# Optimization experiments

Hardware: AMD Instinct MI355X
Metric: run time of the kernel (lower is better)

Reference implementation:

```python
import jax, jax.numpy as jnp
import numpy as np
import math

B, QLEN, KLEN = 8, 128, 1024
KDIM = QDIM = ADIM = ODIM = 512
HM, HC = 4, 4            # monotonic / chunkwise heads
CHUNK = 4                # chunkwise attention window
EPS = 1e-6
SHARPENING = 1.0
NEG_INF = float(np.finfo(np.float32).min)


def moving_sum(x, back, forward):
    """Windowed sum over last axis: out[k] = sum_{j=k-back}^{k+forward} x[j].
    Equivalent to the conv1d-with-ones-filter moving_sum in the torch code."""
    K = x.shape[-1]
    xp = jnp.pad(x, [(0, 0)] * (x.ndim - 1) + [(back, forward)])
    cs = jnp.cumsum(xp, axis=-1)
    L = back + forward + 1
    upper = jax.lax.slice_in_dim(cs, L - 1, L - 1 + K, axis=-1)
    lower = jnp.concatenate([jnp.zeros_like(cs[..., :1]),
                             jax.lax.slice_in_dim(cs, 0, K - 1, axis=-1)], axis=-1)
    return upper - lower


def safe_cumprod(x, eps):
    """exp(exclusive_cumsum(log(clip(x, eps, 1)))) along last axis."""
    logx = jnp.log(jnp.clip(x, eps, 1.0))
    excl = jnp.concatenate([jnp.zeros_like(logx[..., :1]),
                            jnp.cumsum(logx, axis=-1)[..., :-1]], axis=-1)
    return jnp.exp(excl)


def _heads(x, w, b, h):
    y = x @ w + b                                   # [B, L, ADIM]
    bs, L, _ = y.shape
    return y.reshape(bs, L, h, -1).transpose(0, 2, 1, 3)  # [B, h, L, d_k]


def setup_inputs() -> dict:
    key = jax.random.key(0)
    ks = jax.random.split(key, 16)
    s = 0.02
    f32 = jnp.float32
    return {
        "key_x": jax.random.normal(ks[0], (B, KLEN, KDIM), f32),
        "query_x": jax.random.normal(ks[1], (B, QLEN, QDIM), f32),
        "mask": jnp.ones((B, QLEN, KLEN), jnp.int32),
        "wk_m": jax.random.normal(ks[2], (KDIM, ADIM), f32) * s,
        "bk_m": jnp.zeros((ADIM,), f32),
        "wq_m": jax.random.normal(ks[3], (QDIM, ADIM), f32) * s,
        "bq_m": jnp.zeros((ADIM,), f32),
        "r": jnp.asarray(-4.0, f32),
        "wk_c": jax.random.normal(ks[4], (KDIM, ADIM), f32) * s,
        "bk_c": jnp.zeros((ADIM,), f32),
        "wq_c": jax.random.normal(ks[5], (QDIM, ADIM), f32) * s,
        "bq_c": jnp.zeros((ADIM,), f32),
        "wv": jax.random.normal(ks[6], (KDIM, ADIM), f32) * s,
        "bv": jnp.zeros((ADIM,), f32),
        "wo": jax.random.normal(ks[7], (ADIM, ODIM), f32) * s,
        "bo": jnp.zeros((ODIM,), f32),
    }


def reference(key_x, query_x, mask, wk_m, bk_m, wq_m, bq_m, r,
              wk_c, bk_c, wq_c, bq_c, wv, bv, wo, bo):
    scale = math.sqrt(ADIM)
    m = (mask[:, None] > 0)                                    # [B,1,Q,K]

    # ---- monotonic energy (scaled_dot + offset r) ----
    km = _heads(key_x, wk_m, bk_m, HM)                         # [B,HM,K,dk]
    qm = _heads(query_x, wq_m, bq_m, HM)                       # [B,HM,Q,dk]
    e_mono = jnp.einsum('bhqd,bhkd->bhqk', qm, km) / scale + r
    e_mono = jnp.where(m, e_mono, NEG_INF)

    # ---- monotonic alpha via safe_cumprod + per-step cumsum recurrence ----
    p_choose = jax.nn.sigmoid(e_mono)                          # [B,HM,Q,K]
    cp = safe_cumprod(1.0 - p_choose, EPS)                     # [B,HM,Q,K]
    aw0 = jnp.zeros((B, HM, KLEN), e_mono.dtype).at[..., 0].set(1.0)

    def step(aw_prev, pc):
        p_i, cp_i = pc                                         # [B,HM,K]
        aw = p_i * cp_i * jnp.cumsum(aw_prev / jnp.maximum(cp_i, EPS), axis=-1)
        return aw, aw

    _, alpha = jax.lax.scan(step, aw0,
                            (p_choose.transpose(2, 0, 1, 3),
                             cp.transpose(2, 0, 1, 3)))
    alpha = alpha.transpose(1, 2, 0, 3)                        # [B,HM,Q,K]

    # ---- chunkwise energy ----
    kc = _heads(key_x, wk_c, bk_c, HC)
    qc = _heads(query_x, wq_c, bq_c, HC)
    e_chunk = jnp.einsum('bhqd,bhkd->bhqk', qc, kc) / scale
    e_chunk = jnp.where(m, e_chunk, NEG_INF)

    # ---- efficient chunkwise attention (clipped-logit trick) ----
    e = e_chunk - jnp.max(e_chunk, axis=-1, keepdims=True)
    sexp = jnp.maximum(jnp.exp(e), 1e-5)[:, None]              # [B,1,HC,Q,K]
    denom = moving_sum(sexp, CHUNK - 1, 0)                     # [B,1,HC,Q,K]
    beta = sexp * moving_sum(alpha[:, :, None] * SHARPENING / denom,
                             0, CHUNK - 1)                     # [B,HM,HC,Q,K]
    beta = beta.reshape(B, HM * HC, QLEN, KLEN)

    # ---- context + output projection ----
    v = (key_x @ wv + bv).reshape(B, KLEN, HM * HC, ADIM // (HM * HC))
    cv = jnp.einsum('bhqk,bkhd->bqhd', beta, v).reshape(B, QLEN, ADIM)
    return cv @ wo + bo
```

## Files before the change

kernel.cpp:

```cpp
#include <hip/hip_runtime.h>
#include <hip/hip_bf16.h>


#define NEG_INF (-3.402823466e38f)
#define EPS_MOCHA 1e-6f
#define INV_SCALE 0.04419417382415922f

typedef _Float16 half8 __attribute__((ext_vector_type(8)));
typedef _Float16 half4v __attribute__((ext_vector_type(4)));
typedef float f32x4 __attribute__((ext_vector_type(4)));

#define WAITBAR(N) asm volatile("s_waitcnt vmcnt(" #N ") lgkmcnt(0)\n\ts_barrier" ::: "memory")

__device__ __forceinline__ float wave_incl_scan(float x)
{
    int v;
    v = __builtin_amdgcn_update_dpp(0, __builtin_bit_cast(int, x), 0x111, 0xF, 0xF, false);
    x += __builtin_bit_cast(float, v);
    v = __builtin_amdgcn_update_dpp(0, __builtin_bit_cast(int, x), 0x112, 0xF, 0xF, false);
    x += __builtin_bit_cast(float, v);
    v = __builtin_amdgcn_update_dpp(0, __builtin_bit_cast(int, x), 0x114, 0xF, 0xF, false);
    x += __builtin_bit_cast(float, v);
    v = __builtin_amdgcn_update_dpp(0, __builtin_bit_cast(int, x), 0x118, 0xF, 0xF, false);
    x += __builtin_bit_cast(float, v);
    v = __builtin_amdgcn_update_dpp(0, __builtin_bit_cast(int, x), 0x142, 0xA, 0xF, false);
    x += __builtin_bit_cast(float, v);
    v = __builtin_amdgcn_update_dpp(0, __builtin_bit_cast(int, x), 0x143, 0xC, 0xF, false);
    x += __builtin_bit_cast(float, v);
    return x;
}

__device__ __forceinline__ half8 cvt8(float4 a, float4 b)
{
    half8 h = {(_Float16)a.x, (_Float16)a.y, (_Float16)a.z, (_Float16)a.w,
               (_Float16)b.x, (_Float16)b.y, (_Float16)b.z, (_Float16)b.w};
    return h;
}

__global__ __launch_bounds__(256) void cvt_x(
    const float* __restrict__ key_x, const float* __restrict__ query_x,
    _Float16* __restrict__ X16)
{
    const size_t KELEMS = (size_t)8192 * 512;
    size_t o = ((size_t)blockIdx.x * 256 + threadIdx.x) * 8;
    const float* s = (o < KELEMS) ? (key_x + o) : (query_x + (o - KELEMS));
    float4 a = *(const float4*)s;
    float4 b = *(const float4*)(s + 4);
    *(half8*)(X16 + o) = cvt8(a, b);
}

__global__ __launch_bounds__(256) void prep_weights(
    const float* __restrict__ wk_m, const float* __restrict__ wk_c,
    const float* __restrict__ wv, const float* __restrict__ wq_m,
    const float* __restrict__ wq_c, const float* __restrict__ wo,
    _Float16* __restrict__ Wt5, _Float16* __restrict__ Wt_wo)
{
    __shared__ float T[64][65];
    const int z = blockIdx.z;
    const float* W = (z == 0) ? wk_m : (z == 1) ? wk_c : (z == 2) ? wv
                   : (z == 3) ? wq_m : (z == 4) ? wq_c : wo;
    _Float16* O = (z < 5) ? (Wt5 + (size_t)z * 262144) : Wt_wo;
    const int n0 = blockIdx.x * 64, k0 = blockIdx.y * 64;
    const int t = threadIdx.x;
    const int rr = t >> 4, cc = (t & 15) * 4;
#pragma unroll
    for (int r = 0; r < 4; ++r) {
        int k = r * 16 + rr;
        float4 v = *(const float4*)(W + (size_t)(k0 + k) * 512 + n0 + cc);
        T[k][cc + 0] = v.x; T[k][cc + 1] = v.y;
        T[k][cc + 2] = v.z; T[k][cc + 3] = v.w;
    }
    __syncthreads();
    const int nn = t >> 2, kc = (t & 3) * 16;
    _Float16 tmp[16];
#pragma unroll
    for (int i = 0; i < 16; ++i) tmp[i] = (_Float16)T[kc + i][nn];
    _Float16* Op = O + (size_t)(n0 + nn) * 512 + k0 + kc;
    *(half8*)(Op)     = *(half8*)&tmp[0];
    *(half8*)(Op + 8) = *(half8*)&tmp[8];
}

__device__ __forceinline__ void stage16(const _Float16* src, _Float16* dst)
{
    __builtin_amdgcn_global_load_lds(
        (const __attribute__((address_space(1))) void*)src,
        (__attribute__((address_space(3))) void*)dst, 16, 0, 0);
}

template <int NSTEPS>
__device__ __forceinline__ void gemm8_f16(
    const _Float16* __restrict__ Abase, const _Float16* __restrict__ Bbase,
    _Float16* As, _Float16* Bs, f32x4 acc[4][2])
{
    const int tid = threadIdx.x;
    const int lane = tid & 63, wave = tid >> 6;
    const int wm = wave >> 2, wn = wave & 3;
    const int col = lane & 15, quad = lane >> 4;
    const int r0 = tid >> 2, seg = tid & 3;

    const _Float16* Ag = Abase + (size_t)r0 * 512 + seg * 8;
    const _Float16* Bg = Bbase + (size_t)r0 * 512 + seg * 8;

    stage16(Ag, As + tid * 8);
    stage16(Bg, Bs + tid * 8);
    if (NSTEPS > 1) {
        stage16(Ag + 32, As + 4096 + tid * 8);
        stage16(Bg + 32, Bs + 4096 + tid * 8);
        WAITBAR(2);
    } else {
        WAITBAR(0);
    }

#pragma unroll
    for (int ks = 0; ks < NSTEPS; ++ks) {
        const int cur = ks % 3;
        if (ks + 2 < NSTEPS) {
            const int s2 = (ks + 2) % 3;
            stage16(Ag + (ks + 2) * 32, As + s2 * 4096 + tid * 8);
            stage16(Bg + (ks + 2) * 32, Bs + s2 * 4096 + tid * 8);
        }
        const _Float16* Afr = As + cur * 4096 + (size_t)(wm * 64 + col) * 32 + quad * 8;
        const _Float16* Bfr = Bs + cur * 4096 + (size_t)(wn * 32 + col) * 32 + quad * 8;
        half8 a[4], b[2];
#pragma unroll
        for (int t = 0; t < 4; ++t) a[t] = *(const half8*)(Afr + (size_t)t * 16 * 32);
#pragma unroll
        for (int t = 0; t < 2; ++t) b[t] = *(const half8*)(Bfr + (size_t)t * 16 * 32);
#pragma unroll
        for (int mt = 0; mt < 4; ++mt)
#pragma unroll
            for (int nt = 0; nt < 2; ++nt)
                acc[mt][nt] = __builtin_amdgcn_mfma_f32_16x16x32_f16(
                    a[mt], b[nt], acc[mt][nt], 0, 0, 0);
        if (ks + 2 < NSTEPS)      WAITBAR(2);
        else if (ks + 1 < NSTEPS) WAITBAR(0);
    }
}

__device__ __forceinline__ void proj_epilogue8(
    f32x4 acc[4][2], const float* __restrict__ bias, void* __restrict__ Cv,
    int m0, int n0, int f16o)
{
    const int tid = threadIdx.x;
    const int lane = tid & 63, wave = tid >> 6;
    const int wm = wave >> 2, wn = wave & 3;
    const int col = lane & 15, quad = lane >> 4;
    float bnt[2];
#pragma unroll
    for (int nt = 0; nt < 2; ++nt)
        bnt[nt] = bias[n0 + wn * 32 + nt * 16 + col];
#pragma unroll
    for (int mt = 0; mt < 4; ++mt) {
        const int rowb = m0 + wm * 64 + mt * 16 + quad * 4;
#pragma unroll
        for (int nt = 0; nt < 2; ++nt) {
            const int cc = n0 + wn * 32 + nt * 16 + col;
#pragma unroll
            for (int r = 0; r < 4; ++r) {
                float v = acc[mt][nt][r] + bnt[nt];
                if (f16o)
                    ((_Float16*)Cv)[(size_t)(rowb + r) * 512 + cc] = (_Float16)v;
                else
                    ((float*)Cv)[(size_t)(rowb + r) * 512 + cc] = v;
            }
        }
    }
}

__global__ __launch_bounds__(512, 8) void mfma_proj5(
    const _Float16* __restrict__ X16, const _Float16* __restrict__ Wt5,
    const float* __restrict__ b0, void* __restrict__ C0,
    const float* __restrict__ b1, void* __restrict__ C1,
    const float* __restrict__ b2, void* __restrict__ C2,
    const float* __restrict__ b3, void* __restrict__ C3,
    const float* __restrict__ b4, void* __restrict__ C4)
{
    __shared__ _Float16 As[12288];
    __shared__ _Float16 Bs[12288];
    const int bid = (blockIdx.x & 7) * 104 + (blockIdx.x >> 3);
    int g, mblk, nblk;
    if (bid < 768) {
        g = bid >> 8; mblk = (bid & 255) >> 2; nblk = bid & 3;
    } else {
        const int t = bid - 768;
        g = 3 + (t >> 5); mblk = (t & 31) >> 2; nblk = t & 3;
    }
    const bool qry = g >= 3;
    const _Float16* A = X16 + (qry ? (size_t)8192 * 512 : 0);
    const _Float16* Wt = Wt5 + (size_t)g * 262144;
    const float* bias = (g == 0) ? b0 : (g == 1) ? b1 : (g == 2) ? b2
                      : (g == 3) ? b3 : b4;
    void* Cv = (g == 0) ? C0 : (g == 1) ? C1 : (g == 2) ? C2
             : (g == 3) ? C3 : C4;
    const int f16o = (g == 2) ? 0 : 1;
    const int m0 = mblk * 128, n0 = nblk * 128;

    f32x4 acc[4][2];
#pragma unroll
    for (int mt = 0; mt < 4; ++mt)
#pragma unroll
        for (int nt = 0; nt < 2; ++nt) acc[mt][nt] = (f32x4)0.f;
    gemm8_f16<16>(A + (size_t)m0 * 512, Wt + (size_t)n0 * 512, As, Bs, acc);
    proj_epilogue8(acc, bias, Cv, m0, n0, f16o);
}

__global__ __launch_bounds__(512, 4) void mfma_proj_out(
    const _Float16* __restrict__ A16, const _Float16* __restrict__ Wt,
    const float* __restrict__ bias, float* __restrict__ C)
{
    __shared__ _Float16 As[12288];
    __shared__ _Float16 Bs[12288];
    const int m0 = blockIdx.x * 128, n0 = blockIdx.y * 128;
    f32x4 acc[4][2];
#pragma unroll
    for (int mt = 0; mt < 4; ++mt)
#pragma unroll
        for (int nt = 0; nt < 2; ++nt) acc[mt][nt] = (f32x4)0.f;
    gemm8_f16<16>(A16 + (size_t)m0 * 512, Wt + (size_t)n0 * 512, As, Bs, acc);
    proj_epilogue8(acc, bias, C, m0, n0, 0);
}

__global__ __launch_bounds__(512, 4) void energy_mfma(
    const _Float16* __restrict__ Qm, const _Float16* __restrict__ Km,
    const _Float16* __restrict__ Qc, const _Float16* __restrict__ Kc,
    const int* __restrict__ mask, float* __restrict__ e_mono,
    _Float16* __restrict__ e_chunk16, const float* __restrict__ r_ptr)
{
    __shared__ _Float16 As[12288];
    __shared__ _Float16 Bs[12288];
    const int tid = threadIdx.x;
    const int lane = tid & 63, wave = tid >> 6;
    const int wm = wave >> 2, wn = wave & 3;
    const int col = lane & 15, quad = lane >> 4;
    const int kt0 = blockIdx.x * 128;
    const int h = blockIdx.y;
    const int b = blockIdx.z;
    const float rv = r_ptr[0];
    const int r0 = tid >> 2, seg = tid & 3;

    const _Float16* Am0 = Qm + (size_t)(b * 128) * 512 + h * 128 + (size_t)r0 * 512 + seg * 8;
    const _Float16* Ac0 = Qc + (size_t)(b * 128) * 512 + h * 128 + (size_t)r0 * 512 + seg * 8;
    const _Float16* Bm0 = Km + (size_t)(b * 1024 + kt0) * 512 + h * 128 + (size_t)r0 * 512 + seg * 8;
    const _Float16* Bc0 = Kc + (size_t)(b * 1024 + kt0) * 512 + h * 128 + (size_t)r0 * 512 + seg * 8;
#define EGA(s) (((s) < 4 ? Am0 : Ac0) + ((s) & 3) * 32)
#define EGB(s) (((s) < 4 ? Bm0 : Bc0) + ((s) & 3) * 32)

    f32x4 accM[4][2], accC[4][2];
#pragma unroll
    for (int mt = 0; mt < 4; ++mt)
#pragma unroll
        for (int nt = 0; nt < 2; ++nt) { accM[mt][nt] = (f32x4)0.f; accC[mt][nt] = (f32x4)0.f; }

#pragma unroll
    for (int s = 0; s < 2; ++s) {
        stage16(EGA(s), As + s * 4096 + tid * 8);
        stage16(EGB(s), Bs + s * 4096 + tid * 8);
    }
    WAITBAR(2);

#pragma unroll
    for (int ks = 0; ks < 8; ++ks) {
        const int cur = ks % 3;
        if (ks + 2 < 8) {
            const int s2 = (ks + 2) % 3;
            stage16(EGA(ks + 2), As + s2 * 4096 + tid * 8);
            stage16(EGB(ks + 2), Bs + s2 * 4096 + tid * 8);
        }
        const _Float16* Afr = As + cur * 4096 + (size_t)(wm * 64 + col) * 32 + quad * 8;
        const _Float16* Bfr = Bs + cur * 4096 + (size_t)(wn * 32 + col) * 32 + quad * 8;
        half8 a[4], bf[2];
#pragma unroll
        for (int t = 0; t < 4; ++t) a[t]  = *(const half8*)(Afr + (size_t)t * 16 * 32);
#pragma unroll
        for (int t = 0; t < 2; ++t) bf[t] = *(const half8*)(Bfr + (size_t)t * 16 * 32);
        if (ks < 4) {
#pragma unroll
            for (int mt = 0; mt < 4; ++mt)
#pragma unroll
                for (int nt = 0; nt < 2; ++nt)
                    accM[mt][nt] = __builtin_amdgcn_mfma_f32_16x16x32_f16(a[mt], bf[nt], accM[mt][nt], 0, 0, 0);
        } else {
#pragma unroll
            for (int mt = 0; mt < 4; ++mt)
#pragma unroll
                for (int nt = 0; nt < 2; ++nt)
                    accC[mt][nt] = __builtin_amdgcn_mfma_f32_16x16x32_f16(a[mt], bf[nt], accC[mt][nt], 0, 0, 0);
        }
        if (ks + 2 < 8)      WAITBAR(2);
        else if (ks + 1 < 8) WAITBAR(0);
    }
#undef EGA
#undef EGB

#pragma unroll
    for (int mt = 0; mt < 4; ++mt) {
        const int qb = wm * 64 + mt * 16 + quad * 4;
#pragma unroll
        for (int nt = 0; nt < 2; ++nt) {
            const int kc = kt0 + wn * 32 + nt * 16 + col;
#pragma unroll
            for (int r = 0; r < 4; ++r) {
                const int q = qb + r;
                const int mv = mask[((size_t)b * 128 + q) * 1024 + kc];
                const size_t oi = (((size_t)b * 4 + h) * 128 + q) * 1024 + kc;
                float vm = accM[mt][nt][r] * INV_SCALE + rv;
                e_mono[oi] = mv ? vm : NEG_INF;
                float vc = accC[mt][nt][r] * INV_SCALE;
                e_chunk16[oi] = (_Float16)(mv ? vc : NEG_INF);
            }
        }
    }
}

__device__ __forceinline__ void transcend_row(
    const float* __restrict__ Erow, int lane, float o_pcp[16], float o_inv[16])
{
    const float* E = Erow + lane * 16;
    float e[16];
    *(float4*)&e[0]  = *(const float4*)(E);
    *(float4*)&e[4]  = *(const float4*)(E + 4);
    *(float4*)&e[8]  = *(const float4*)(E + 8);
    *(float4*)&e[12] = *(const float4*)(E + 12);

    float p[16], l[16];
#pragma unroll
    for (int i = 0; i < 16; ++i) {
        p[i] = 1.f / (1.f + expf(-e[i]));
        l[i] = logf(fmaxf(1.f - p[i], EPS_MOCHA));
    }
    float incl[16];
    incl[0] = l[0];
#pragma unroll
    for (int i = 1; i < 16; ++i) incl[i] = incl[i - 1] + l[i];
    float total = incl[15];
    float x = wave_incl_scan(total);
    float base = x - total;
#pragma unroll
    for (int i = 0; i < 16; ++i) {
        float cl = base + (i ? incl[i - 1] : 0.f);
        float cp = expf(cl);
        o_pcp[i] = p[i] * cp;
        o_inv[i] = 1.f / fmaxf(cp, EPS_MOCHA);
    }
}

#define SW2(k) ((k) + ((k) >> 4))

__global__ __launch_bounds__(256) void alpha_pre(
    const float* __restrict__ e_mono, float* __restrict__ G,
    float* __restrict__ pcp)
{
    __shared__ float pshare[4][1088];
    const int tid = threadIdx.x;
    const int lane = tid & 63;
    const int wid = tid >> 6;
    const int row = blockIdx.x * 4 + wid;
    const int q = row & 127;

    float pq[16], iq[16];
    transcend_row(e_mono + (size_t)row * 1024, lane, pq, iq);

    float* P = pcp + (size_t)row * 1024 + lane * 16;
    *(float4*)(P)      = *(float4*)&pq[0];
    *(float4*)(P + 4)  = *(float4*)&pq[4];
    *(float4*)(P + 8)  = *(float4*)&pq[8];
    *(float4*)(P + 12) = *(float4*)&pq[12];

#pragma unroll
    for (int i = 0; i < 16; ++i)
        pshare[wid][SW2(lane * 16 + i)] = pq[i];
    __syncthreads();

    float g[16];
    if (q == 0) {
#pragma unroll
        for (int i = 0; i < 16; ++i) g[i] = 0.f;
        if (lane == 0) g[0] = iq[0];
    } else if (wid > 0) {
#pragma unroll
        for (int i = 0; i < 16; ++i)
            g[i] = pshare[wid - 1][SW2(lane * 16 + i)] * iq[i];
    } else {
        float pm[16], im[16];
        transcend_row(e_mono + (size_t)(row - 1) * 1024, lane, pm, im);
#pragma unroll
        for (int i = 0; i < 16; ++i) g[i] = pm[i] * iq[i];
    }
    float* Gp = G + (size_t)row * 1024 + lane * 16;
    *(float4*)(Gp)      = *(float4*)&g[0];
    *(float4*)(Gp + 4)  = *(float4*)&g[4];
    *(float4*)(Gp + 8)  = *(float4*)&g[8];
    *(float4*)(Gp + 12) = *(float4*)&g[12];
}

__global__ __launch_bounds__(64, 1) void alpha_scan(
    const float* __restrict__ G, float* __restrict__ S)
{
    const int lane = threadIdx.x;
    const int bh = blockIdx.x;
    const float* Gp = G + (size_t)bh * 131072 + lane * 16;
    float* Sp = S + (size_t)bh * 131072 + lane * 16;

    float bg[8][16];
#pragma unroll
    for (int s = 0; s < 8; ++s) {
        const float* Gq = Gp + (size_t)s * 1024;
        *(float4*)&bg[s][0]  = *(const float4*)(Gq);
        *(float4*)&bg[s][4]  = *(const float4*)(Gq + 4);
        *(float4*)&bg[s][8]  = *(const float4*)(Gq + 8);
        *(float4*)&bg[s][12] = *(const float4*)(Gq + 12);
    }

    float Sv[16];
#pragma unroll
    for (int i = 0; i < 16; ++i) Sv[i] = 1.f;

    for (int q8 = 0; q8 < 128; q8 += 8) {
#pragma unroll
        for (int s = 0; s < 8; ++s) {
            const int q = q8 + s;
            float g[16];
#pragma unroll
            for (int i = 0; i < 16; ++i) g[i] = bg[s][i];
            if (q + 8 < 128) {
                const float* Gq = Gp + (size_t)(q + 8) * 1024;
                *(float4*)&bg[s][0]  = *(const float4*)(Gq);
                *(float4*)&bg[s][4]  = *(const float4*)(Gq + 4);
                *(float4*)&bg[s][8]  = *(const float4*)(Gq + 8);
                *(float4*)&bg[s][12] = *(const float4*)(Gq + 12);
            }

            float incl[16];
            incl[0] = g[0] * Sv[0];
#pragma unroll
            for (int i = 1; i < 16; ++i)
                incl[i] = fmaf(g[i], Sv[i], incl[i - 1]);
            float total = incl[15];
            float x = wave_incl_scan(total);
            float base = x - total;
#pragma unroll
            for (int i = 0; i < 16; ++i) Sv[i] = base + incl[i];

            float* Sq = Sp + (size_t)q * 1024;
            *(float4*)(Sq)      = *(float4*)&Sv[0];
            *(float4*)(Sq + 4)  = *(float4*)&Sv[4];
            *(float4*)(Sq + 8)  = *(float4*)&Sv[8];
            *(float4*)(Sq + 12) = *(float4*)&Sv[12];
        }
    }
}

__global__ __launch_bounds__(256) void beta_kernel(
    const _Float16* __restrict__ e_chunk16, const float* __restrict__ pcp,
    const float* __restrict__ S, _Float16* __restrict__ beta)
{
    __shared__ float red[4];
    __shared__ float edge_sx[4][4];
    __shared__ float edge_t[4][4][4];
    const int q = blockIdx.x, b = blockIdx.y;
    const int tid = threadIdx.x;
    const int lane = tid & 63, wid = tid >> 6;
    const int k4 = tid * 4;

    float av[4][4];
#pragma unroll
    for (int hm = 0; hm < 4; ++hm) {
        const size_t off = (((size_t)b * 4 + hm) * 128 + q) * 1024 + k4;
        float4 pv = *(const float4*)(pcp + off);
        float4 sv = *(const float4*)(S + off);
        av[hm][0] = pv.x * sv.x;
        av[hm][1] = pv.y * sv.y;
        av[hm][2] = pv.z * sv.z;
        av[hm][3] = pv.w * sv.w;
    }

    for (int hc = 0; hc < 4; ++hc) {
        half4v ev = *(const half4v*)(e_chunk16 + (((size_t)b * 4 + hc) * 128 + q) * 1024 + k4);
        float e[4] = {(float)ev[0], (float)ev[1], (float)ev[2], (float)ev[3]};

        float mx = fmaxf(fmaxf(e[0], e[1]), fmaxf(e[2], e[3]));
#pragma unroll
        for (int off = 32; off >= 1; off >>= 1)
            mx = fmaxf(mx, __shfl_xor(mx, off, 64));
        if (lane == 0) red[wid] = mx;
        __syncthreads();
        mx = fmaxf(fmaxf(red[0], red[1]), fmaxf(red[2], red[3]));

        float sx[4];
#pragma unroll
        for (int i = 0; i < 4; ++i)
            sx[i] = fmaxf(expf(e[i] - mx), 1e-5f);
        if (lane == 63) {
            edge_sx[wid][0] = sx[0]; edge_sx[wid][1] = sx[1];
            edge_sx[wid][2] = sx[2]; edge_sx[wid][3] = sx[3];
        }
        __syncthreads();

        float p1 = __shfl_up(sx[3], 1, 64);
        float p2 = __shfl_up(sx[2], 1, 64);
        float p3 = __shfl_up(sx[1], 1, 64);
        if (lane == 0) {
            if (wid > 0) {
                p1 = edge_sx[wid - 1][3];
                p2 = edge_sx[wid - 1][2];
                p3 = edge_sx[wid - 1][1];
            } else {
                p1 = 0.f; p2 = 0.f; p3 = 0.f;
            }
        }
        float den[4];
        den[0] = sx[0] + p1 + p2 + p3;
        den[1] = sx[1] + sx[0] + p1 + p2;
        den[2] = sx[2] + sx[1] + sx[0] + p1;
        den[3] = sx[3] + sx[2] + sx[1] + sx[0];

        float t[4][4];
#pragma unroll
        for (int hm = 0; hm < 4; ++hm)
#pragma unroll
            for (int i = 0; i < 4; ++i)
                t[hm][i] = av[hm][i] / den[i];
        if (lane == 0) {
#pragma unroll
            for (int hm = 0; hm < 4; ++hm) {
                edge_t[wid][hm][0] = t[hm][0]; edge_t[wid][hm][1] = t[hm][1];
                edge_t[wid][hm][2] = t[hm][2]; edge_t[wid][hm][3] = t[hm][3];
            }
        }
        __syncthreads();

#pragma unroll
        for (int hm = 0; hm < 4; ++hm) {
            float n1 = __shfl_down(t[hm][0], 1, 64);
            float n2 = __shfl_down(t[hm][1], 1, 64);
            float n3 = __shfl_down(t[hm][2], 1, 64);
            if (lane == 63) {
                if (wid < 3) {
                    n1 = edge_t[wid + 1][hm][0];
                    n2 = edge_t[wid + 1][hm][1];
                    n3 = edge_t[wid + 1][hm][2];
                } else {
                    n1 = 0.f; n2 = 0.f; n3 = 0.f;
                }
            }
            float o0 = sx[0] * (t[hm][0] + t[hm][1] + t[hm][2] + t[hm][3]);
            float o1 = sx[1] * (t[hm][1] + t[hm][2] + t[hm][3] + n1);
            float o2 = sx[2] * (t[hm][2] + t[hm][3] + n1 + n2);
            float o3 = sx[3] * (t[hm][3] + n1 + n2 + n3);
            _Float16* Brow = beta + (((size_t)b * 16 + hm * 4 + hc) * 128 + q) * 1024;
            half4v hv = {(_Float16)o0, (_Float16)o1, (_Float16)o2, (_Float16)o3};
            *(half4v*)(Brow + k4) = hv;
        }
    }
}

__global__ __launch_bounds__(256) void context_kernel(
    const _Float16* __restrict__ beta, const float* __restrict__ V,
    _Float16* __restrict__ cv16)
{
    __shared__ float bS[128][64];
    __shared__ float vS[128][32];
    const int qh = blockIdx.x, h = blockIdx.y, b = blockIdx.z;
    const int tid = threadIdx.x;
    const int ty = tid >> 3, tx = tid & 7;
    const int q0 = qh * 64;

    const _Float16* Bbase = beta + (((size_t)b * 16 + h) * 128 + q0) * 1024;
    const float* Vbase = V + (size_t)b * 1024 * 512 + h * 32;

    float acc[2][4];
#pragma unroll
    for (int i = 0; i < 2; ++i)
#pragma unroll
        for (int j = 0; j < 4; ++j) acc[i][j] = 0.f;

    for (int k0 = 0; k0 < 1024; k0 += 128) {
        {
            int r = tid >> 2, c = tid & 3;
#pragma unroll
            for (int s = 0; s < 4; ++s) {
                half8 v = *(const half8*)(Bbase + (size_t)r * 1024 + k0 + s * 32 + c * 8);
#pragma unroll
                for (int j = 0; j < 8; ++j) bS[s * 32 + c * 8 + j][r] = (float)v[j];
            }
        }
        {
            int kk = tid >> 3, c = tid & 7;
#pragma unroll
            for (int s = 0; s < 4; ++s) {
                float4 v = *(const float4*)(Vbase + (size_t)(k0 + s * 32 + kk) * 512 + c * 4);
                *(float4*)&vS[s * 32 + kk][c * 4] = v;
            }
        }
        __syncthreads();
#pragma unroll 8
        for (int kk = 0; kk < 128; ++kk) {
            float a0 = bS[kk][ty * 2], a1 = bS[kk][ty * 2 + 1];
            float bb[4];
            *(float4*)bb = *(const float4*)&vS[kk][tx * 4];
#pragma unroll
            for (int j = 0; j < 4; ++j) {
                acc[0][j] = fmaf(a0, bb[j], acc[0][j]);
                acc[1][j] = fmaf(a1, bb[j], acc[1][j]);
            }
        }
        __syncthreads();
    }
#pragma unroll
    for (int i = 0; i < 2; ++i) {
        _Float16* Cp = cv16 + ((size_t)b * 128 + q0 + ty * 2 + i) * 512 + h * 32 + tx * 4;
        half4v hv = {(_Float16)acc[i][0], (_Float16)acc[i][1],
                     (_Float16)acc[i][2], (_Float16)acc[i][3]};
        *(half4v*)Cp = hv;
    }
}

extern "C" void kernel_launch(void* const* d_in, const int* in_sizes, int n_in,
                              void* d_out, int out_size, void* d_ws, size_t ws_size,
                              hipStream_t stream)
{
    const float* key_x   = (const float*)d_in[0];
    const float* query_x = (const float*)d_in[1];
    const int*   mask    = (const int*)d_in[2];
    const float* wk_m = (const float*)d_in[3];
    const float* bk_m = (const float*)d_in[4];
    const float* wq_m = (const float*)d_in[5];
    const float* bq_m = (const float*)d_in[6];
    const float* r    = (const float*)d_in[7];
    const float* wk_c = (const float*)d_in[8];
    const float* bk_c = (const float*)d_in[9];
    const float* wq_c = (const float*)d_in[10];
    const float* bq_c = (const float*)d_in[11];
    const float* wv   = (const float*)d_in[12];
    const float* bv   = (const float*)d_in[13];
    const float* wo   = (const float*)d_in[14];
    const float* bo   = (const float*)d_in[15];
    float* out = (float*)d_out;

    float* ws = (float*)d_ws;
    _Float16* hws = (_Float16*)d_ws;
    const size_t MEGF = 1024 * 1024;
    _Float16* Km16  = hws;
    _Float16* Kc16  = hws + 4 * MEGF;
    _Float16* Qm16  = hws + 8 * MEGF;
    _Float16* Qc16  = hws + 8 * MEGF + 524288;
    _Float16* X16   = hws + 16 * MEGF;
    float* e_mono  = ws + 11 * MEGF;
    _Float16* e_chunk16 = hws + 34 * MEGF;
    float* V       = ws + 19 * MEGF;
    float* G       = ws;
    float* pcp     = ws + 4 * MEGF;
    float* S       = ws + 23 * MEGF;
    _Float16* beta16 = hws + 16 * MEGF;
    _Float16* Wt5   = hws + 54 * MEGF;
    _Float16* Wt_wo = hws + 54 * MEGF + 5 * 262144;
    _Float16* cv16  = hws + 55 * MEGF + MEGF / 2;

    cvt_x<<<dim3(2304), 256, 0, stream>>>(key_x, query_x, X16);
    prep_weights<<<dim3(8, 8, 6), 256, 0, stream>>>(
        wk_m, wk_c, wv, wq_m, wq_c, wo, Wt5, Wt_wo);
    mfma_proj5<<<dim3(832), 512, 0, stream>>>(
        X16, Wt5, bk_m, Km16, bk_c, Kc16, bv, V, bq_m, Qm16, bq_c, Qc16);
    energy_mfma<<<dim3(8, 4, 8), 512, 0, stream>>>(
        Qm16, Km16, Qc16, Kc16, mask, e_mono, e_chunk16, r);
    alpha_pre<<<dim3(1024), 256, 0, stream>>>(e_mono, G, pcp);
    alpha_scan<<<dim3(32), 64, 0, stream>>>(G, S);
    beta_kernel<<<dim3(128, 8), 256, 0, stream>>>(e_chunk16, pcp, S, beta16);
    context_kernel<<<dim3(2, 16, 8), 256, 0, stream>>>(beta16, V, cv16);
    mfma_proj_out<<<dim3(8, 4), 512, 0, stream>>>(cv16, Wt_wo, bo, out);
}
```

Baseline: 252.4 us.

## Merge prep kernels, store V in fp16, fold alpha product into scan, fast math

After: 255.8 us. No clear change (+1.3%).

```diff
diff --git a/kernel.cpp b/kernel.cpp
--- a/kernel.cpp
+++ b/kernel.cpp
@@ -11,6 +11,8 @@
 typedef float f32x4 __attribute__((ext_vector_type(4)));
 
 #define WAITBAR(N) asm volatile("s_waitcnt vmcnt(" #N ") lgkmcnt(0)\n\ts_barrier" ::: "memory")
+
+__device__ __forceinline__ float frcp(float x) { return __builtin_amdgcn_rcpf(x); }
 
 __device__ __forceinline__ float wave_incl_scan(float x)
 {
@@ -37,47 +39,47 @@
     return h;
 }
 
-__global__ __launch_bounds__(256) void cvt_x(
-    const float* __restrict__ key_x, const float* __restrict__ query_x,
-    _Float16* __restrict__ X16)
-{
-    const size_t KELEMS = (size_t)8192 * 512;
-    size_t o = ((size_t)blockIdx.x * 256 + threadIdx.x) * 8;
-    const float* s = (o < KELEMS) ? (key_x + o) : (query_x + (o - KELEMS));
-    float4 a = *(const float4*)s;
-    float4 b = *(const float4*)(s + 4);
-    *(half8*)(X16 + o) = cvt8(a, b);
-}
-
-__global__ __launch_bounds__(256) void prep_weights(
+__global__ __launch_bounds__(256) void prep_all(
     const float* __restrict__ wk_m, const float* __restrict__ wk_c,
     const float* __restrict__ wv, const float* __restrict__ wq_m,
     const float* __restrict__ wq_c, const float* __restrict__ wo,
-    _Float16* __restrict__ Wt5, _Float16* __restrict__ Wt_wo)
+    const float* __restrict__ key_x, const float* __restrict__ query_x,
+    _Float16* __restrict__ Wt5, _Float16* __restrict__ Wt_wo,
+    _Float16* __restrict__ X16)
 {
     __shared__ float T[64][65];
-    const int z = blockIdx.z;
-    const float* W = (z == 0) ? wk_m : (z == 1) ? wk_c : (z == 2) ? wv
-                   : (z == 3) ? wq_m : (z == 4) ? wq_c : wo;
-    _Float16* O = (z < 5) ? (Wt5 + (size_t)z * 262144) : Wt_wo;
-    const int n0 = blockIdx.x * 64, k0 = blockIdx.y * 64;
+    const int bid = blockIdx.x;
     const int t = threadIdx.x;
-    const int rr = t >> 4, cc = (t & 15) * 4;
-#pragma unroll
-    for (int r = 0; r < 4; ++r) {
-        int k = r * 16 + rr;
-        float4 v = *(const float4*)(W + (size_t)(k0 + k) * 512 + n0 + cc);
-        T[k][cc + 0] = v.x; T[k][cc + 1] = v.y;
-        T[k][cc + 2] = v.z; T[k][cc + 3] = v.w;
-    }
-    __syncthreads();
-    const int nn = t >> 2, kc = (t & 3) * 16;
-    _Float16 tmp[16];
-#pragma unroll
-    for (int i = 0; i < 16; ++i) tmp[i] = (_Float16)T[kc + i][nn];
-    _Float16* Op = O + (size_t)(n0 + nn) * 512 + k0 + kc;
-    *(half8*)(Op)     = *(half8*)&tmp[0];
-    *(half8*)(Op + 8) = *(half8*)&tmp[8];
+    if (bid < 384) {
+        const int z = bid >> 6, w = bid & 63;
+        const float* W = (z == 0) ? wk_m : (z == 1) ? wk_c : (z == 2) ? wv
+                       : (z == 3) ? wq_m : (z == 4) ? wq_c : wo;
+        _Float16* O = (z < 5) ? (Wt5 + (size_t)z * 262144) : Wt_wo;
+        const int n0 = (w & 7) * 64, k0 = (w >> 3) * 64;
+        const int rr = t >> 4, cc = (t & 15) * 4;
+#pragma unroll
+        for (int r = 0; r < 4; ++r) {
+            int k = r * 16 + rr;
+            float4 v = *(const float4*)(W + (size_t)(k0 + k) * 512 + n0 + cc);
+            T[k][cc + 0] = v.x; T[k][cc + 1] = v.y;
+            T[k][cc + 2] = v.z; T[k][cc + 3] = v.w;
+        }
+        __syncthreads();
+        const int nn = t >> 2, kc = (t & 3) * 16;
+        _Float16 tmp[16];
+#pragma unroll
+        for (int i = 0; i < 16; ++i) tmp[i] = (_Float16)T[kc + i][nn];
+        _Float16* Op = O + (size_t)(n0 + nn) * 512 + k0 + kc;
+        *(half8*)(Op)     = *(half8*)&tmp[0];
+        *(half8*)(Op + 8) = *(half8*)&tmp[8];
+    } else {
+        const size_t KELEMS = (size_t)8192 * 512;
+        size_t o = ((size_t)(bid - 384) * 256 + t) * 8;
+        const float* s = (o < KELEMS) ? (key_x + o) : (query_x + (o - KELEMS));
+        float4 a = *(const float4*)s;
+        float4 b = *(const float4*)(s + 4);
+        *(half8*)(X16 + o) = cvt8(a, b);
+    }
 }
 
 __device__ __forceinline__ void stage16(const _Float16* src, _Float16* dst)
@@ -192,7 +194,6 @@
                       : (g == 3) ? b3 : b4;
     void* Cv = (g == 0) ? C0 : (g == 1) ? C1 : (g == 2) ? C2
              : (g == 3) ? C3 : C4;
-    const int f16o = (g == 2) ? 0 : 1;
     const int m0 = mblk * 128, n0 = nblk * 128;
 
     f32x4 acc[4][2];
@@ -201,7 +202,7 @@
 #pragma unroll
         for (int nt = 0; nt < 2; ++nt) acc[mt][nt] = (f32x4)0.f;
     gemm8_f16<16>(A + (size_t)m0 * 512, Wt + (size_t)n0 * 512, As, Bs, acc);
-    proj_epilogue8(acc, bias, Cv, m0, n0, f16o);
+    proj_epilogue8(acc, bias, Cv, m0, n0, 1);
 }
 
 __global__ __launch_bounds__(512, 4) void mfma_proj_out(
@@ -325,8 +326,8 @@
     float p[16], l[16];
 #pragma unroll
     for (int i = 0; i < 16; ++i) {
-        p[i] = 1.f / (1.f + expf(-e[i]));
-        l[i] = logf(fmaxf(1.f - p[i], EPS_MOCHA));
+        p[i] = frcp(1.f + __expf(-e[i]));
+        l[i] = __logf(fmaxf(1.f - p[i], EPS_MOCHA));
     }
     float incl[16];
     incl[0] = l[0];
@@ -338,23 +339,23 @@
 #pragma unroll
     for (int i = 0; i < 16; ++i) {
         float cl = base + (i ? incl[i - 1] : 0.f);
-        float cp = expf(cl);
+        float cp = __expf(cl);
         o_pcp[i] = p[i] * cp;
-        o_inv[i] = 1.f / fmaxf(cp, EPS_MOCHA);
+        o_inv[i] = frcp(fmaxf(cp, EPS_MOCHA));
     }
 }
 
 #define SW2(k) ((k) + ((k) >> 4))
 
-__global__ __launch_bounds__(256) void alpha_pre(
+__global__ __launch_bounds__(512) void alpha_pre(
     const float* __restrict__ e_mono, float* __restrict__ G,
     float* __restrict__ pcp)
 {
-    __shared__ float pshare[4][1088];
+    __shared__ float pshare[8][1088];
     const int tid = threadIdx.x;
     const int lane = tid & 63;
     const int wid = tid >> 6;
-    const int row = blockIdx.x * 4 + wid;
+    const int row = blockIdx.x * 8 + wid;
     const int q = row & 127;
 
     float pq[16], iq[16];
@@ -394,21 +395,28 @@
 }
 
 __global__ __launch_bounds__(64, 1) void alpha_scan(
-    const float* __restrict__ G, float* __restrict__ S)
+    const float* __restrict__ G, const float* __restrict__ pcp,
+    float* __restrict__ alpha)
 {
     const int lane = threadIdx.x;
     const int bh = blockIdx.x;
     const float* Gp = G + (size_t)bh * 131072 + lane * 16;
-    float* Sp = S + (size_t)bh * 131072 + lane * 16;
-
-    float bg[8][16];
+    const float* Pp = pcp + (size_t)bh * 131072 + lane * 16;
+    float* Ap = alpha + (size_t)bh * 131072 + lane * 16;
+
+    float bg[8][16], bp[8][16];
 #pragma unroll
     for (int s = 0; s < 8; ++s) {
         const float* Gq = Gp + (size_t)s * 1024;
+        const float* Pq = Pp + (size_t)s * 1024;
         *(float4*)&bg[s][0]  = *(const float4*)(Gq);
         *(float4*)&bg[s][4]  = *(const float4*)(Gq + 4);
         *(float4*)&bg[s][8]  = *(const float4*)(Gq + 8);
         *(float4*)&bg[s][12] = *(const float4*)(Gq + 12);
+        *(float4*)&bp[s][0]  = *(const float4*)(Pq);
+        *(float4*)&bp[s][4]  = *(const float4*)(Pq + 4);
+        *(float4*)&bp[s][8]  = *(const float4*)(Pq + 8);
+        *(float4*)&bp[s][12] = *(const float4*)(Pq + 12);
     }
 
     float Sv[16];
@@ -419,15 +427,20 @@
 #pragma unroll
         for (int s = 0; s < 8; ++s) {
             const int q = q8 + s;
-            float g[16];
-#pragma unroll
-            for (int i = 0; i < 16; ++i) g[i] = bg[s][i];
+            float g[16], pv[16];
+#pragma unroll
+            for (int i = 0; i < 16; ++i) { g[i] = bg[s][i]; pv[i] = bp[s][i]; }
             if (q + 8 < 128) {
                 const float* Gq = Gp + (size_t)(q + 8) * 1024;
+                const float* Pq = Pp + (size_t)(q + 8) * 1024;
                 *(float4*)&bg[s][0]  = *(const float4*)(Gq);
                 *(float4*)&bg[s][4]  = *(const float4*)(Gq + 4);
                 *(float4*)&bg[s][8]  = *(const float4*)(Gq + 8);
                 *(float4*)&bg[s][12] = *(const float4*)(Gq + 12);
+                *(float4*)&bp[s][0]  = *(const float4*)(Pq);
+                *(float4*)&bp[s][4]  = *(const float4*)(Pq + 4);
+                *(float4*)&bp[s][8]  = *(const float4*)(Pq + 8);
+                *(float4*)&bp[s][12] = *(const float4*)(Pq + 12);
             }
 
             float incl[16];
@@ -441,18 +454,21 @@
 #pragma unroll
             for (int i = 0; i < 16; ++i) Sv[i] = base + incl[i];
 
-            float* Sq = Sp + (size_t)q * 1024;
-            *(float4*)(Sq)      = *(float4*)&Sv[0];
-            *(float4*)(Sq + 4)  = *(float4*)&Sv[4];
-            *(float4*)(Sq + 8)  = *(float4*)&Sv[8];
-            *(float4*)(Sq + 12) = *(float4*)&Sv[12];
+            float av[16];
+#pragma unroll
+            for (int i = 0; i < 16; ++i) av[i] = pv[i] * Sv[i];
+            float* Aq = Ap + (size_t)q * 1024;
+            *(float4*)(Aq)      = *(float4*)&av[0];
+            *(float4*)(Aq + 4)  = *(float4*)&av[4];
+            *(float4*)(Aq + 8)  = *(float4*)&av[8];
+            *(float4*)(Aq + 12) = *(float4*)&av[12];
         }
     }
 }
 
 __global__ __launch_bounds__(256) void beta_kernel(
-    const _Float16* __restrict__ e_chunk16, const float* __restrict__ pcp,
-    const float* __restrict__ S, _Float16* __restrict__ beta)
+    const _Float16* __restrict__ e_chunk16, const float* __restrict__ alpha,
+    _Float16* __restrict__ beta)
 {
     __shared__ float red[4];
     __shared__ float edge_sx[4][4];
@@ -466,12 +482,8 @@
 #pragma unroll
     for (int hm = 0; hm < 4; ++hm) {
         const size_t off = (((size_t)b * 4 + hm) * 128 + q) * 1024 + k4;
-        float4 pv = *(const float4*)(pcp + off);
-        float4 sv = *(const float4*)(S + off);
-        av[hm][0] = pv.x * sv.x;
-        av[hm][1] = pv.y * sv.y;
-        av[hm][2] = pv.z * sv.z;
-        av[hm][3] = pv.w * sv.w;
+        float4 a = *(const float4*)(alpha + off);
+        av[hm][0] = a.x; av[hm][1] = a.y; av[hm][2] = a.z; av[hm][3] = a.w;
     }
 
     for (int hc = 0; hc < 4; ++hc) {
@@ -489,7 +501,7 @@
         float sx[4];
 #pragma unroll
         for (int i = 0; i < 4; ++i)
-            sx[i] = fmaxf(expf(e[i] - mx), 1e-5f);
+            sx[i] = fmaxf(__expf(e[i] - mx), 1e-5f);
         if (lane == 63) {
             edge_sx[wid][0] = sx[0]; edge_sx[wid][1] = sx[1];
             edge_sx[wid][2] = sx[2]; edge_sx[wid][3] = sx[3];
@@ -513,13 +525,16 @@
         den[1] = sx[1] + sx[0] + p1 + p2;
         den[2] = sx[2] + sx[1] + sx[0] + p1;
         den[3] = sx[3] + sx[2] + sx[1] + sx[0];
+        float rd[4];
+#pragma unroll
+        for (int i = 0; i < 4; ++i) rd[i] = frcp(den[i]);
 
         float t[4][4];
 #pragma unroll
         for (int hm = 0; hm < 4; ++hm)
 #pragma unroll
             for (int i = 0; i < 4; ++i)
-                t[hm][i] = av[hm][i] / den[i];
+                t[hm][i] = av[hm][i] * rd[i];
         if (lane == 0) {
 #pragma unroll
             for (int hm = 0; hm < 4; ++hm) {
@@ -555,7 +570,7 @@
 }
 
 __global__ __launch_bounds__(256) void context_kernel(
-    const _Float16* __restrict__ beta, const float* __restrict__ V,
+    const _Float16* __restrict__ beta, const _Float16* __restrict__ V16,
     _Float16* __restrict__ cv16)
 {
     __shared__ float bS[128][64];
@@ -566,7 +581,7 @@
     const int q0 = qh * 64;
 
     const _Float16* Bbase = beta + (((size_t)b * 16 + h) * 128 + q0) * 1024;
-    const float* Vbase = V + (size_t)b * 1024 * 512 + h * 32;
+    const _Float16* Vbase = V16 + (size_t)b * 1024 * 512 + h * 32;
 
     float acc[2][4];
 #pragma unroll
@@ -588,8 +603,9 @@
             int kk = tid >> 3, c = tid & 7;
 #pragma unroll
             for (int s = 0; s < 4; ++s) {
-                float4 v = *(const float4*)(Vbase + (size_t)(k0 + s * 32 + kk) * 512 + c * 4);
-                *(float4*)&vS[s * 32 + kk][c * 4] = v;
+                half4v v = *(const half4v*)(Vbase + (size_t)(k0 + s * 32 + kk) * 512 + c * 4);
+                float4 f = {(float)v[0], (float)v[1], (float)v[2], (float)v[3]};
+                *(float4*)&vS[s * 32 + kk][c * 4] = f;
             }
         }
         __syncthreads();
@@ -647,25 +663,24 @@
     _Float16* X16   = hws + 16 * MEGF;
     float* e_mono  = ws + 11 * MEGF;
     _Float16* e_chunk16 = hws + 34 * MEGF;
-    float* V       = ws + 19 * MEGF;
+    _Float16* V16  = hws + 38 * MEGF;
     float* G       = ws;
     float* pcp     = ws + 4 * MEGF;
-    float* S       = ws + 23 * MEGF;
+    float* alpha   = ws + 23 * MEGF;
     _Float16* beta16 = hws + 16 * MEGF;
     _Float16* Wt5   = hws + 54 * MEGF;
     _Float16* Wt_wo = hws + 54 * MEGF + 5 * 262144;
     _Float16* cv16  = hws + 55 * MEGF + MEGF / 2;
 
-    cvt_x<<<dim3(2304), 256, 0, stream>>>(key_x, query_x, X16);
-    prep_weights<<<dim3(8, 8, 6), 256, 0, stream>>>(
-        wk_m, wk_c, wv, wq_m, wq_c, wo, Wt5, Wt_wo);
+    prep_all<<<dim3(2688), 256, 0, stream>>>(
+        wk_m, wk_c, wv, wq_m, wq_c, wo, key_x, query_x, Wt5, Wt_wo, X16);
     mfma_proj5<<<dim3(832), 512, 0, stream>>>(
-        X16, Wt5, bk_m, Km16, bk_c, Kc16, bv, V, bq_m, Qm16, bq_c, Qc16);
+        X16, Wt5, bk_m, Km16, bk_c, Kc16, bv, V16, bq_m, Qm16, bq_c, Qc16);
     energy_mfma<<<dim3(8, 4, 8), 512, 0, stream>>>(
         Qm16, Km16, Qc16, Kc16, mask, e_mono, e_chunk16, r);
-    alpha_pre<<<dim3(1024), 256, 0, stream>>>(e_mono, G, pcp);
-    alpha_scan<<<dim3(32), 64, 0, stream>>>(G, S);
-    beta_kernel<<<dim3(128, 8), 256, 0, stream>>>(e_chunk16, pcp, S, beta16);
-    context_kernel<<<dim3(2, 16, 8), 256, 0, stream>>>(beta16, V, cv16);
+    alpha_pre<<<dim3(512), 512, 0, stream>>>(e_mono, G, pcp);
+    alpha_scan<<<dim3(32), 64, 0, stream>>>(G, pcp, alpha);
+    beta_kernel<<<dim3(128, 8), 256, 0, stream>>>(e_chunk16, alpha, beta16);
+    context_kernel<<<dim3(2, 16, 8), 256, 0, stream>>>(beta16, V16, cv16);
     mfma_proj_out<<<dim3(8, 4), 512, 0, stream>>>(cv16, Wt_wo, bo, out);
 }
```
